# Kernel optimization log

Measured on AMD Instinct MI355X. Metric: run time of the kernel, lower is better.

The kernel has to match this reference:

```python
import jax, jax.numpy as jnp
import numpy as np

N_NODES = 50000
N_EDGES = 800000
F_IN, F_HID, F_OUT = 128, 256, 256


def setup_inputs() -> dict:
    key = jax.random.key(0)
    ks = jax.random.split(key, 8)
    x = jax.random.normal(ks[0], (N_NODES, F_IN), dtype=jnp.float32)
    edge_index = jax.random.randint(ks[1], (2, N_EDGES), 0, N_NODES, dtype=jnp.int64)

    def lin(k, fan_in, fan_out):
        return jax.random.normal(k, (fan_in, fan_out), dtype=jnp.float32) / np.sqrt(fan_in).astype(np.float32)

    return {
        "x": x,
        "edge_index": edge_index,
        "W1": lin(ks[2], F_IN, F_HID),  "b1": jnp.zeros((F_HID,), jnp.float32),
        "W2": lin(ks[3], F_HID, F_HID), "b2": jnp.zeros((F_HID,), jnp.float32),
        "W3": lin(ks[4], F_HID, F_OUT), "b3": jnp.zeros((F_OUT,), jnp.float32),
    }


def reference(x, edge_index, W1, b1, W2, b2, W3, b3):
    # GCN (eval mode): edge_drop and feature dropout are identity; bn=False.
    n = x.shape[0]
    loops = jnp.arange(n, dtype=edge_index.dtype)
    src = jnp.concatenate([edge_index[0], loops])  # [E+N] with self-loops
    dst = jnp.concatenate([edge_index[1], loops])

    # Symmetric normalization deg^{-1/2}[src] * deg^{-1/2}[dst] (deg over dst incl. self-loops)
    deg = jax.ops.segment_sum(jnp.ones_like(dst, dtype=x.dtype), dst, num_segments=n)
    dinv = jnp.where(deg > 0, jax.lax.rsqrt(deg), jnp.zeros_like(deg))
    norm = dinv[src] * dinv[dst]  # [E+N]

    def gcn_conv(h, W, b):
        h = h @ W                                       # [N, out]
        msg = h[src] * norm[:, None]                    # gather + scale  [E+N, out]
        return jax.ops.segment_sum(msg, dst, num_segments=n) + b  # scatter-add

    h = jax.nn.relu(gcn_conv(x, W1, b1))
    h = jax.nn.relu(gcn_conv(h, W2, b2))
    return gcn_conv(h, W3, b3)
```

## Files before the change

kernel.cpp:

```cpp
#include <hip/hip_runtime.h>
#include <hip/hip_bf16.h>

#define NNODES 50000
#define NEDGES 800000
#define F_IN 128
#define F_HID 256

using u16 = unsigned short;
using u32 = unsigned int;
using f32x4 = __attribute__((ext_vector_type(4))) float;
using s16x8 = __attribute__((ext_vector_type(8))) short;

constexpr int SCAN_BLOCKS = (NNODES + 255) / 256;
constexpr int B2SHIFT = 9;
constexpr int NB2 = (NNODES + 511) >> 9;
constexpr int NBLK = 256;
constexpr int EPB = NEDGES / NBLK;

constexpr size_t OFF_DINV   = 0;
constexpr size_t OFF_ROWPTR = 200192;
constexpr size_t OFF_CNT    = 400384;
constexpr size_t OFF_BSUM   = 600576;
constexpr size_t OFF_BSUMS  = 601600;
constexpr size_t OFF_CMAT   = 602624;
constexpr size_t OFF_PAIRS  = 702976;
constexpr size_t OFF_PW     = 3902976;
constexpr size_t OFF_XB     = 7102976;
constexpr size_t OFF_HB     = 19902976;
constexpr size_t OFF_AGGB   = 45502976;
constexpr size_t OFF_W1T    = 71102976;
constexpr size_t OFF_W2T    = 71168512;
constexpr size_t OFF_W3T    = 71299584;

static __device__ __forceinline__ float b2f(u16 u) {
    union { unsigned int i; float f; } v;
    v.i = ((unsigned int)u) << 16;
    return v.f;
}
static __device__ __forceinline__ u16 f2b(float f) {
    __hip_bfloat16 h = __float2bfloat16(f);
    return __builtin_bit_cast(u16, h);
}

static __device__ __forceinline__ bool detect_wide(const void* raw) {
    __shared__ int bad;
    if (threadIdx.x == 0) bad = 0;
    __syncthreads();
    unsigned long long v = ((const unsigned long long*)raw)[threadIdx.x & 255];
    if (v >= (unsigned long long)NNODES) atomicAdd(&bad, 1);
    __syncthreads();
    return bad == 0;
}

__global__ __launch_bounds__(256) void hist_kernel(const void* __restrict__ raw,
                                                   int* __restrict__ cnt, int* __restrict__ cmat) {
    const bool wide = detect_wide(raw);
    __shared__ int h[NB2];
    int t = threadIdx.x;
    if (t < NB2) h[t] = 0;
    __syncthreads();
    const int base = blockIdx.x * EPB;
    for (int i = t; i < EPB; i += 256) {
        int e = base + i;
        int d = wide ? (int)((const long long*)raw)[NEDGES + e] : ((const int*)raw)[NEDGES + e];
        atomicAdd(&h[d >> B2SHIFT], 1);
        atomicAdd(&cnt[d], 1);
    }
    __syncthreads();
    if (t < NB2) cmat[t * NBLK + blockIdx.x] = h[t];
}

__global__ __launch_bounds__(256) void offset_kernel(const int* __restrict__ row_ptr, int* __restrict__ cmat) {
    __shared__ int s[256];
    int b = blockIdx.x;
    int t = threadIdx.x;
    int v = cmat[b * NBLK + t];
    s[t] = v;
    __syncthreads();
    for (int o = 1; o < 256; o <<= 1) {
        int tmp = (t >= o) ? s[t - o] : 0;
        __syncthreads();
        s[t] += tmp;
        __syncthreads();
    }
    cmat[b * NBLK + t] = row_ptr[b << B2SHIFT] + s[t] - v;
}

__global__ __launch_bounds__(256) void scatter_kernel(const void* __restrict__ raw,
                                                      const int* __restrict__ cmat,
                                                      u32* __restrict__ pairs) {
    const bool wide = detect_wide(raw);
    __shared__ int cur[NB2];
    int t = threadIdx.x;
    if (t < NB2) cur[t] = cmat[t * NBLK + blockIdx.x];
    __syncthreads();
    const int base = blockIdx.x * EPB;
    for (int i = t; i < EPB; i += 256) {
        int e = base + i;
        int s, d;
        if (wide) {
            const long long* p = (const long long*)raw;
            s = (int)p[e];
            d = (int)p[NEDGES + e];
        } else {
            const int* p = (const int*)raw;
            s = p[e];
            d = p[NEDGES + e];
        }
        int pos = atomicAdd(&cur[d >> B2SHIFT], 1);
        pairs[pos] = ((u32)(d & 511) << 16) | (u32)s;
    }
}

__global__ __launch_bounds__(256) void phase2_fill(const u32* __restrict__ pairs,
                                                   const int* __restrict__ row_ptr,
                                                   const float* __restrict__ dinv,
                                                   u32* __restrict__ pw) {
    __shared__ int lcnt[512];
    __shared__ int lbase[512];
    int b = blockIdx.x;
    int n0 = b << B2SHIFT;
    int t = threadIdx.x;
    for (int i = t; i < 512; i += 256) {
        lcnt[i] = 0;
        int nd = n0 + i;
        lbase[i] = (nd < NNODES) ? row_ptr[nd] : NEDGES;
    }
    __syncthreads();
    int hi = n0 + 512; if (hi > NNODES) hi = NNODES;
    int p0 = row_ptr[n0];
    int p1 = row_ptr[hi];
    for (int p = p0 + t; p < p1; p += 256) {
        u32 pk = pairs[p];
        int dl = (int)(pk >> 16);
        int src = (int)(pk & 0xFFFFu);
        int r = atomicAdd(&lcnt[dl], 1);
        u16 wb = f2b(dinv[src]);
        pw[lbase[dl] + r] = ((u32)wb << 16) | (u32)src;
    }
}

__global__ __launch_bounds__(256) void scan_reduce(const int* __restrict__ cnt, int* __restrict__ bsum,
                                                   float* __restrict__ dinv) {
    __shared__ int s[256];
    int i = blockIdx.x * 256 + threadIdx.x;
    int c = (i < NNODES) ? cnt[i] : 0;
    if (i < NNODES) dinv[i] = rsqrtf((float)c + 1.0f);
    s[threadIdx.x] = c;
    __syncthreads();
    for (int o = 128; o > 0; o >>= 1) {
        if (threadIdx.x < o) s[threadIdx.x] += s[threadIdx.x + o];
        __syncthreads();
    }
    if (threadIdx.x == 0) bsum[blockIdx.x] = s[0];
}

__global__ __launch_bounds__(256) void scan_top(const int* __restrict__ bsum, int* __restrict__ bsumS) {
    __shared__ int s[256];
    int t = threadIdx.x;
    int v = (t < SCAN_BLOCKS) ? bsum[t] : 0;
    s[t] = v;
    __syncthreads();
    for (int o = 1; o < 256; o <<= 1) {
        int tmp = (t >= o) ? s[t - o] : 0;
        __syncthreads();
        s[t] += tmp;
        __syncthreads();
    }
    if (t < SCAN_BLOCKS) bsumS[t] = s[t] - v;
}

__global__ __launch_bounds__(256) void scan_final(const int* __restrict__ cnt, const int* __restrict__ bsumS,
                                                  int* __restrict__ row_ptr) {
    __shared__ int s[256];
    int t = threadIdx.x;
    int i = blockIdx.x * 256 + t;
    int v = (i < NNODES) ? cnt[i] : 0;
    s[t] = v;
    __syncthreads();
    for (int o = 1; o < 256; o <<= 1) {
        int tmp = (t >= o) ? s[t - o] : 0;
        __syncthreads();
        s[t] += tmp;
        __syncthreads();
    }
    if (i < NNODES) row_ptr[i] = s[t] - v + bsumS[blockIdx.x];
    if (i == 0) row_ptr[NNODES] = NEDGES;
}

__global__ __launch_bounds__(256) void convert_all(const float* __restrict__ x,
                                                   const float* __restrict__ W1, const float* __restrict__ W2,
                                                   const float* __restrict__ W3, u16* __restrict__ xb,
                                                   u16* __restrict__ W1t, u16* __restrict__ W2t,
                                                   u16* __restrict__ W3t) {
    int bid = blockIdx.x;
    if (bid < 6250) {
        int i = bid * 256 + threadIdx.x;
        float4 v = ((const float4*)x)[i];
        ushort4 o;
        o.x = f2b(v.x); o.y = f2b(v.y); o.z = f2b(v.z); o.w = f2b(v.w);
        ((ushort4*)xb)[i] = o;
    } else {
        int idx = (bid - 6250) * 256 + threadIdx.x;
        if (idx < 32768) {
            int k = idx >> 8, n = idx & 255;
            W1t[n * 128 + k] = f2b(W1[idx]);
        } else if (idx < 98304) {
            int j = idx - 32768;
            int k = j >> 8, n = j & 255;
            W2t[n * 256 + k] = f2b(W2[j]);
        } else {
            int j = idx - 98304;
            int k = j >> 8, n = j & 255;
            W3t[n * 256 + k] = f2b(W3[j]);
        }
    }
}

template <int F>
__global__ __launch_bounds__(256) void agg_kernel(const u16* __restrict__ h,
                                                  const int* __restrict__ row_ptr,
                                                  const u32* __restrict__ pw,
                                                  const float* __restrict__ dinv,
                                                  u16* __restrict__ outb) {
    constexpr int VEC = F / 64;
    int lane = threadIdx.x & 63;
    int v = __builtin_amdgcn_readfirstlane((int)(blockIdx.x * 4 + (threadIdx.x >> 6)));
    const size_t lo = (size_t)lane * VEC;

    const int e0 = row_ptr[v], e1 = row_ptr[v + 1];
    float dv = dinv[v];
    float acc[VEC];
    {
        const u16* p = h + (size_t)v * F + lo;
        if constexpr (VEC == 4) {
            ushort4 t = *(const ushort4*)p;
            acc[0] = dv * b2f(t.x); acc[1] = dv * b2f(t.y); acc[2] = dv * b2f(t.z); acc[3] = dv * b2f(t.w);
        } else {
            ushort2 t = *(const ushort2*)p;
            acc[0] = dv * b2f(t.x); acc[1] = dv * b2f(t.y);
        }
    }
    for (int e = e0; e < e1; e += 8) {
        u32 pk[8];
#pragma unroll
        for (int u = 0; u < 8; ++u) {
            int idx = e + u;
            pk[u] = pw[idx < e1 ? idx : e1 - 1];
        }
        int   c[8];
        float w[8];
#pragma unroll
        for (int u = 0; u < 8; ++u) {
            c[u] = (int)(pk[u] & 0xFFFFu);
            w[u] = (e + u < e1) ? b2f((u16)(pk[u] >> 16)) : 0.0f;
        }
        if constexpr (VEC == 4) {
            ushort4 r[8];
#pragma unroll
            for (int u = 0; u < 8; ++u)
                r[u] = *(const ushort4*)(h + (size_t)c[u] * F + lo);
#pragma unroll
            for (int u = 0; u < 8; ++u) {
                acc[0] += w[u] * b2f(r[u].x);
                acc[1] += w[u] * b2f(r[u].y);
                acc[2] += w[u] * b2f(r[u].z);
                acc[3] += w[u] * b2f(r[u].w);
            }
        } else {
            ushort2 r[8];
#pragma unroll
            for (int u = 0; u < 8; ++u)
                r[u] = *(const ushort2*)(h + (size_t)c[u] * F + lo);
#pragma unroll
            for (int u = 0; u < 8; ++u) {
                acc[0] += w[u] * b2f(r[u].x);
                acc[1] += w[u] * b2f(r[u].y);
            }
        }
    }
    u16* o = outb + (size_t)v * F + lo;
    if constexpr (VEC == 4) {
        ushort4 t;
        t.x = f2b(dv * acc[0]); t.y = f2b(dv * acc[1]); t.z = f2b(dv * acc[2]); t.w = f2b(dv * acc[3]);
        *(ushort4*)o = t;
    } else {
        ushort2 t;
        t.x = f2b(dv * acc[0]); t.y = f2b(dv * acc[1]);
        *(ushort2*)o = t;
    }
}

template <int KT, bool RELU, bool OUT_BF16>
__global__ __launch_bounds__(256) void gemm_mfma(const u16* __restrict__ A, const u16* __restrict__ Wt,
                                                 const float* __restrict__ bias, void* __restrict__ outp,
                                                 int M) {
    constexpr int BM = 128, BN = 128, BK = 32;
    __shared__ __align__(16) u16 As[BM * BK];
    __shared__ __align__(16) u16 Bs[BN * BK];
    const int tid = threadIdx.x;
    const int lane = tid & 63, wid = tid >> 6;
    const int l15 = lane & 15, lhi = lane >> 4;
    const int m0 = blockIdx.x * BM, n0 = blockIdx.y * BN;
    const int wr = (wid >> 1) * 64, wc = (wid & 1) * 64;

    f32x4 acc[4][4] = {};

    const int sr = tid >> 1;
    const int sc2 = (tid & 1) * 2;

    for (int k0 = 0; k0 < KT; k0 += BK) {
        uint4 av0, av1, bv0, bv1;
        int ar = m0 + sr;
        if (ar < M) {
            const uint4* ap = (const uint4*)(A + (size_t)ar * KT + k0 + sc2 * 8);
            av0 = ap[0]; av1 = ap[1];
        } else {
            av0 = make_uint4(0, 0, 0, 0); av1 = av0;
        }
        const uint4* bp = (const uint4*)(Wt + (size_t)(n0 + sr) * KT + k0 + sc2 * 8);
        bv0 = bp[0]; bv1 = bp[1];

        __syncthreads();
        *(uint4*)&As[sr * BK + ((sc2 ^ (sr & 3)) * 8)]       = av0;
        *(uint4*)&As[sr * BK + (((sc2 + 1) ^ (sr & 3)) * 8)] = av1;
        *(uint4*)&Bs[sr * BK + ((sc2 ^ (sr & 3)) * 8)]       = bv0;
        *(uint4*)&Bs[sr * BK + (((sc2 + 1) ^ (sr & 3)) * 8)] = bv1;
        __syncthreads();

        s16x8 af[4], bfr[4];
#pragma unroll
        for (int m = 0; m < 4; ++m) {
            int r = wr + m * 16 + l15;
            af[m] = *(const s16x8*)&As[r * BK + ((lhi ^ (r & 3)) * 8)];
        }
#pragma unroll
        for (int n = 0; n < 4; ++n) {
            int r = wc + n * 16 + l15;
            bfr[n] = *(const s16x8*)&Bs[r * BK + ((lhi ^ (r & 3)) * 8)];
        }
#pragma unroll
        for (int m = 0; m < 4; ++m)
#pragma unroll
            for (int n = 0; n < 4; ++n)
                acc[m][n] = __builtin_amdgcn_mfma_f32_16x16x32_bf16(af[m], bfr[n], acc[m][n], 0, 0, 0);
    }

#pragma unroll
    for (int n = 0; n < 4; ++n) {
        int gcol = n0 + wc + n * 16 + l15;
        float bb = bias[gcol];
#pragma unroll
        for (int m = 0; m < 4; ++m) {
            int gr0 = m0 + wr + m * 16 + lhi * 4;
#pragma unroll
            for (int r = 0; r < 4; ++r) {
                int gr = gr0 + r;
                if (gr >= M) continue;
                float vv = acc[m][n][r] + bb;
                if (RELU) vv = vv > 0.f ? vv : 0.f;
                if (OUT_BF16)
                    ((u16*)outp)[(size_t)gr * 256 + gcol] = f2b(vv);
                else
                    ((float*)outp)[(size_t)gr * 256 + gcol] = vv;
            }
        }
    }
}

extern "C" void kernel_launch(void* const* d_in, const int* in_sizes, int n_in,
                              void* d_out, int out_size, void* d_ws, size_t ws_size,
                              hipStream_t stream) {
    const float* x  = (const float*)d_in[0];
    const void* edges = d_in[1];
    const float* W1 = (const float*)d_in[2];
    const float* b1 = (const float*)d_in[3];
    const float* W2 = (const float*)d_in[4];
    const float* b2 = (const float*)d_in[5];
    const float* W3 = (const float*)d_in[6];
    const float* b3 = (const float*)d_in[7];
    float* out = (float*)d_out;

    char* ws = (char*)d_ws;
    float* dinv   = (float*)(ws + OFF_DINV);
    int*   rowptr = (int*)(ws + OFF_ROWPTR);
    int*   cnt    = (int*)(ws + OFF_CNT);
    int*   bsum   = (int*)(ws + OFF_BSUM);
    int*   bsumS  = (int*)(ws + OFF_BSUMS);
    int*   cmat   = (int*)(ws + OFF_CMAT);
    u32*   pairs  = (u32*)(ws + OFF_PAIRS);
    u32*   pw     = (u32*)(ws + OFF_PW);
    u16*   xb     = (u16*)(ws + OFF_XB);
    u16*   hb     = (u16*)(ws + OFF_HB);
    u16*   aggb   = (u16*)(ws + OFF_AGGB);
    u16*   W1t    = (u16*)(ws + OFF_W1T);
    u16*   W2t    = (u16*)(ws + OFF_W2T);
    u16*   W3t    = (u16*)(ws + OFF_W3T);

    hipMemsetAsync(cnt, 0, NNODES * sizeof(int), stream);

    hist_kernel<<<NBLK, 256, 0, stream>>>(edges, cnt, cmat);

    scan_reduce<<<SCAN_BLOCKS, 256, 0, stream>>>(cnt, bsum, dinv);
    scan_top<<<1, 256, 0, stream>>>(bsum, bsumS);
    scan_final<<<SCAN_BLOCKS, 256, 0, stream>>>(cnt, bsumS, rowptr);

    offset_kernel<<<NB2, 256, 0, stream>>>(rowptr, cmat);
    scatter_kernel<<<NBLK, 256, 0, stream>>>(edges, cmat, pairs);
    phase2_fill<<<NB2, 256, 0, stream>>>(pairs, rowptr, dinv, pw);

    convert_all<<<6890, 256, 0, stream>>>(x, W1, W2, W3, xb, W1t, W2t, W3t);

    const int AGG_GRID = NNODES / 4;
    dim3 ggrid((NNODES + 127) / 128, 2);

    agg_kernel<F_IN><<<AGG_GRID, 256, 0, stream>>>(xb, rowptr, pw, dinv, aggb);
    gemm_mfma<F_IN, true, true><<<ggrid, 256, 0, stream>>>(aggb, W1t, b1, hb, NNODES);

    agg_kernel<F_HID><<<AGG_GRID, 256, 0, stream>>>(hb, rowptr, pw, dinv, aggb);
    gemm_mfma<F_HID, true, true><<<ggrid, 256, 0, stream>>>(aggb, W2t, b2, hb, NNODES);

    agg_kernel<F_HID><<<AGG_GRID, 256, 0, stream>>>(hb, rowptr, pw, dinv, aggb);
    gemm_mfma<F_HID, false, false><<<ggrid, 256, 0, stream>>>(aggb, W3t, b3, out, NNODES);
}
```

Measured before the change: 316.5 us.

## Derive CSR row pointers from bucket-local counts, drop global degree atomics

Removes the per-node global atomic degree histogram, its memset, and the three-kernel global scan. Row pointers and inverse sqrt degrees are now computed per 512-node bucket from the already-bucketed pairs, using shared-memory counts and a scan, and a small scan over bucket totals supplies the bucket bases. The aggregation inner loop is also unrolled from 8 to 16 edges to keep more gathers in flight, at the cost of more registers. The fill pass now needs a second read of pairs.

```diff
diff --git a/kernel.cpp b/kernel.cpp
--- a/kernel.cpp
+++ b/kernel.cpp
@@ -11,7 +11,6 @@
 using f32x4 = __attribute__((ext_vector_type(4))) float;
 using s16x8 = __attribute__((ext_vector_type(8))) short;
 
-constexpr int SCAN_BLOCKS = (NNODES + 255) / 256;
 constexpr int B2SHIFT = 9;
 constexpr int NB2 = (NNODES + 511) >> 9;
 constexpr int NBLK = 256;
@@ -19,18 +18,17 @@
 
 constexpr size_t OFF_DINV   = 0;
 constexpr size_t OFF_ROWPTR = 200192;
-constexpr size_t OFF_CNT    = 400384;
-constexpr size_t OFF_BSUM   = 600576;
-constexpr size_t OFF_BSUMS  = 601600;
-constexpr size_t OFF_CMAT   = 602624;
-constexpr size_t OFF_PAIRS  = 702976;
-constexpr size_t OFF_PW     = 3902976;
-constexpr size_t OFF_XB     = 7102976;
-constexpr size_t OFF_HB     = 19902976;
-constexpr size_t OFF_AGGB   = 45502976;
-constexpr size_t OFF_W1T    = 71102976;
-constexpr size_t OFF_W2T    = 71168512;
-constexpr size_t OFF_W3T    = 71299584;
+constexpr size_t OFF_CMAT   = 400384;
+constexpr size_t OFF_BTOT   = 500736;
+constexpr size_t OFF_BBASE  = 501760;
+constexpr size_t OFF_PAIRS  = 502784;
+constexpr size_t OFF_PW     = 3702784;
+constexpr size_t OFF_XB     = 6902784;
+constexpr size_t OFF_HB     = 19702784;
+constexpr size_t OFF_AGGB   = 45302784;
+constexpr size_t OFF_W1T    = 70902784;
+constexpr size_t OFF_W2T    = 70968320;
+constexpr size_t OFF_W3T    = 71099392;
 
 static __device__ __forceinline__ float b2f(u16 u) {
     union { unsigned int i; float f; } v;
@@ -52,8 +50,7 @@
     return bad == 0;
 }
 
-__global__ __launch_bounds__(256) void hist_kernel(const void* __restrict__ raw,
-                                                   int* __restrict__ cnt, int* __restrict__ cmat) {
+__global__ __launch_bounds__(256) void hist_kernel(const void* __restrict__ raw, int* __restrict__ cmat) {
     const bool wide = detect_wide(raw);
     __shared__ int h[NB2];
     int t = threadIdx.x;
@@ -64,13 +61,12 @@
         int e = base + i;
         int d = wide ? (int)((const long long*)raw)[NEDGES + e] : ((const int*)raw)[NEDGES + e];
         atomicAdd(&h[d >> B2SHIFT], 1);
-        atomicAdd(&cnt[d], 1);
     }
     __syncthreads();
     if (t < NB2) cmat[t * NBLK + blockIdx.x] = h[t];
 }
 
-__global__ __launch_bounds__(256) void offset_kernel(const int* __restrict__ row_ptr, int* __restrict__ cmat) {
+__global__ __launch_bounds__(256) void offset_kernel(int* __restrict__ cmat, int* __restrict__ btot) {
     __shared__ int s[256];
     int b = blockIdx.x;
     int t = threadIdx.x;
@@ -83,16 +79,33 @@
         s[t] += tmp;
         __syncthreads();
     }
-    cmat[b * NBLK + t] = row_ptr[b << B2SHIFT] + s[t] - v;
+    cmat[b * NBLK + t] = s[t] - v;
+    if (t == 255) btot[b] = s[255];
+}
+
+__global__ void bscan_kernel(const int* __restrict__ btot, int* __restrict__ bbase) {
+    __shared__ int s[128];
+    int t = threadIdx.x;
+    int v = (t < NB2) ? btot[t] : 0;
+    s[t] = v;
+    __syncthreads();
+    for (int o = 1; o < 128; o <<= 1) {
+        int tmp = (t >= o) ? s[t - o] : 0;
+        __syncthreads();
+        s[t] += tmp;
+        __syncthreads();
+    }
+    if (t < NB2) bbase[t] = s[t] - v;
 }
 
 __global__ __launch_bounds__(256) void scatter_kernel(const void* __restrict__ raw,
                                                       const int* __restrict__ cmat,
+                                                      const int* __restrict__ bbase,
                                                       u32* __restrict__ pairs) {
     const bool wide = detect_wide(raw);
     __shared__ int cur[NB2];
     int t = threadIdx.x;
-    if (t < NB2) cur[t] = cmat[t * NBLK + blockIdx.x];
+    if (t < NB2) cur[t] = cmat[t * NBLK + blockIdx.x] + bbase[t];
     __syncthreads();
     const int base = blockIdx.x * EPB;
     for (int i = t; i < EPB; i += 256) {
@@ -112,80 +125,54 @@
     }
 }
 
-__global__ __launch_bounds__(256) void phase2_fill(const u32* __restrict__ pairs,
-                                                   const int* __restrict__ row_ptr,
-                                                   const float* __restrict__ dinv,
-                                                   u32* __restrict__ pw) {
+__global__ __launch_bounds__(256) void phase2a(const u32* __restrict__ pairs,
+                                               const int* __restrict__ bbase, const int* __restrict__ btot,
+                                               int* __restrict__ row_ptr, float* __restrict__ dinv) {
     __shared__ int lcnt[512];
-    __shared__ int lbase[512];
-    int b = blockIdx.x;
+    __shared__ int ssc[512];
+    int b = blockIdx.x, t = threadIdx.x;
     int n0 = b << B2SHIFT;
-    int t = threadIdx.x;
-    for (int i = t; i < 512; i += 256) {
-        lcnt[i] = 0;
-        int nd = n0 + i;
-        lbase[i] = (nd < NNODES) ? row_ptr[nd] : NEDGES;
-    }
-    __syncthreads();
-    int hi = n0 + 512; if (hi > NNODES) hi = NNODES;
-    int p0 = row_ptr[n0];
-    int p1 = row_ptr[hi];
+    lcnt[t] = 0; lcnt[t + 256] = 0;
+    __syncthreads();
+    int p0 = bbase[b], p1 = p0 + btot[b];
+    for (int p = p0 + t; p < p1; p += 256)
+        atomicAdd(&lcnt[pairs[p] >> 16], 1);
+    __syncthreads();
+    int c0 = lcnt[t], c1 = lcnt[t + 256];
+    ssc[t] = c0; ssc[t + 256] = c1;
+    __syncthreads();
+    for (int o = 1; o < 512; o <<= 1) {
+        int a0 = (t >= o) ? ssc[t - o] : 0;
+        int a1 = ssc[t + 256 - o];
+        __syncthreads();
+        ssc[t] += a0; ssc[t + 256] += a1;
+        __syncthreads();
+    }
+    int na = n0 + t, nb = n0 + t + 256;
+    if (na < NNODES) { row_ptr[na] = p0 + ssc[t] - c0;       dinv[na] = rsqrtf((float)c0 + 1.0f); }
+    if (nb < NNODES) { row_ptr[nb] = p0 + ssc[t + 256] - c1; dinv[nb] = rsqrtf((float)c1 + 1.0f); }
+    if (b == 0 && t == 0) row_ptr[NNODES] = NEDGES;
+}
+
+__global__ __launch_bounds__(256) void phase2b(const u32* __restrict__ pairs,
+                                               const int* __restrict__ bbase, const int* __restrict__ btot,
+                                               const int* __restrict__ row_ptr, const float* __restrict__ dinv,
+                                               u32* __restrict__ pw) {
+    __shared__ int lcur[512];
+    int b = blockIdx.x, t = threadIdx.x;
+    int n0 = b << B2SHIFT;
+    int na = n0 + t, nb = n0 + t + 256;
+    lcur[t]       = (na < NNODES) ? row_ptr[na] : NEDGES;
+    lcur[t + 256] = (nb < NNODES) ? row_ptr[nb] : NEDGES;
+    __syncthreads();
+    int p0 = bbase[b], p1 = p0 + btot[b];
     for (int p = p0 + t; p < p1; p += 256) {
         u32 pk = pairs[p];
         int dl = (int)(pk >> 16);
         int src = (int)(pk & 0xFFFFu);
-        int r = atomicAdd(&lcnt[dl], 1);
-        u16 wb = f2b(dinv[src]);
-        pw[lbase[dl] + r] = ((u32)wb << 16) | (u32)src;
-    }
-}
-
-__global__ __launch_bounds__(256) void scan_reduce(const int* __restrict__ cnt, int* __restrict__ bsum,
-                                                   float* __restrict__ dinv) {
-    __shared__ int s[256];
-    int i = blockIdx.x * 256 + threadIdx.x;
-    int c = (i < NNODES) ? cnt[i] : 0;
-    if (i < NNODES) dinv[i] = rsqrtf((float)c + 1.0f);
-    s[threadIdx.x] = c;
-    __syncthreads();
-    for (int o = 128; o > 0; o >>= 1) {
-        if (threadIdx.x < o) s[threadIdx.x] += s[threadIdx.x + o];
-        __syncthreads();
-    }
-    if (threadIdx.x == 0) bsum[blockIdx.x] = s[0];
-}
-
-__global__ __launch_bounds__(256) void scan_top(const int* __restrict__ bsum, int* __restrict__ bsumS) {
-    __shared__ int s[256];
-    int t = threadIdx.x;
-    int v = (t < SCAN_BLOCKS) ? bsum[t] : 0;
-    s[t] = v;
-    __syncthreads();
-    for (int o = 1; o < 256; o <<= 1) {
-        int tmp = (t >= o) ? s[t - o] : 0;
-        __syncthreads();
-        s[t] += tmp;
-        __syncthreads();
-    }
-    if (t < SCAN_BLOCKS) bsumS[t] = s[t] - v;
-}
-
-__global__ __launch_bounds__(256) void scan_final(const int* __restrict__ cnt, const int* __restrict__ bsumS,
-                                                  int* __restrict__ row_ptr) {
-    __shared__ int s[256];
-    int t = threadIdx.x;
-    int i = blockIdx.x * 256 + t;
-    int v = (i < NNODES) ? cnt[i] : 0;
-    s[t] = v;
-    __syncthreads();
-    for (int o = 1; o < 256; o <<= 1) {
-        int tmp = (t >= o) ? s[t - o] : 0;
-        __syncthreads();
-        s[t] += tmp;
-        __syncthreads();
-    }
-    if (i < NNODES) row_ptr[i] = s[t] - v + bsumS[blockIdx.x];
-    if (i == 0) row_ptr[NNODES] = NEDGES;
+        int pos = atomicAdd(&lcur[dl], 1);
+        pw[pos] = ((u32)f2b(dinv[src]) << 16) | (u32)src;
+    }
 }
 
 __global__ __launch_bounds__(256) void convert_all(const float* __restrict__ x,
@@ -241,39 +228,39 @@
             acc[0] = dv * b2f(t.x); acc[1] = dv * b2f(t.y);
         }
     }
-    for (int e = e0; e < e1; e += 8) {
-        u32 pk[8];
-#pragma unroll
-        for (int u = 0; u < 8; ++u) {
+    for (int e = e0; e < e1; e += 16) {
+        u32 pk[16];
+#pragma unroll
+        for (int u = 0; u < 16; ++u) {
             int idx = e + u;
             pk[u] = pw[idx < e1 ? idx : e1 - 1];
         }
-        int   c[8];
-        float w[8];
-#pragma unroll
-        for (int u = 0; u < 8; ++u) {
+        int   c[16];
+        float w[16];
+#pragma unroll
+        for (int u = 0; u < 16; ++u) {
             c[u] = (int)(pk[u] & 0xFFFFu);
             w[u] = (e + u < e1) ? b2f((u16)(pk[u] >> 16)) : 0.0f;
         }
         if constexpr (VEC == 4) {
-            ushort4 r[8];
-#pragma unroll
-            for (int u = 0; u < 8; ++u)
+            ushort4 r[16];
+#pragma unroll
+            for (int u = 0; u < 16; ++u)
                 r[u] = *(const ushort4*)(h + (size_t)c[u] * F + lo);
 #pragma unroll
-            for (int u = 0; u < 8; ++u) {
+            for (int u = 0; u < 16; ++u) {
                 acc[0] += w[u] * b2f(r[u].x);
                 acc[1] += w[u] * b2f(r[u].y);
                 acc[2] += w[u] * b2f(r[u].z);
                 acc[3] += w[u] * b2f(r[u].w);
             }
         } else {
-            ushort2 r[8];
-#pragma unroll
-            for (int u = 0; u < 8; ++u)
+            ushort2 r[16];
+#pragma unroll
+            for (int u = 0; u < 16; ++u)
                 r[u] = *(const ushort2*)(h + (size_t)c[u] * F + lo);
 #pragma unroll
-            for (int u = 0; u < 8; ++u) {
+            for (int u = 0; u < 16; ++u) {
                 acc[0] += w[u] * b2f(r[u].x);
                 acc[1] += w[u] * b2f(r[u].y);
             }
@@ -384,10 +371,9 @@
     char* ws = (char*)d_ws;
     float* dinv   = (float*)(ws + OFF_DINV);
     int*   rowptr = (int*)(ws + OFF_ROWPTR);
-    int*   cnt    = (int*)(ws + OFF_CNT);
-    int*   bsum   = (int*)(ws + OFF_BSUM);
-    int*   bsumS  = (int*)(ws + OFF_BSUMS);
     int*   cmat   = (int*)(ws + OFF_CMAT);
+    int*   btot   = (int*)(ws + OFF_BTOT);
+    int*   bbase  = (int*)(ws + OFF_BBASE);
     u32*   pairs  = (u32*)(ws + OFF_PAIRS);
     u32*   pw     = (u32*)(ws + OFF_PW);
     u16*   xb     = (u16*)(ws + OFF_XB);
@@ -397,17 +383,12 @@
     u16*   W2t    = (u16*)(ws + OFF_W2T);
     u16*   W3t    = (u16*)(ws + OFF_W3T);
 
-    hipMemsetAsync(cnt, 0, NNODES * sizeof(int), stream);
-
-    hist_kernel<<<NBLK, 256, 0, stream>>>(edges, cnt, cmat);
-
-    scan_reduce<<<SCAN_BLOCKS, 256, 0, stream>>>(cnt, bsum, dinv);
-    scan_top<<<1, 256, 0, stream>>>(bsum, bsumS);
-    scan_final<<<SCAN_BLOCKS, 256, 0, stream>>>(cnt, bsumS, rowptr);
-
-    offset_kernel<<<NB2, 256, 0, stream>>>(rowptr, cmat);
-    scatter_kernel<<<NBLK, 256, 0, stream>>>(edges, cmat, pairs);
-    phase2_fill<<<NB2, 256, 0, stream>>>(pairs, rowptr, dinv, pw);
+    hist_kernel<<<NBLK, 256, 0, stream>>>(edges, cmat);
+    offset_kernel<<<NB2, 256, 0, stream>>>(cmat, btot);
+    bscan_kernel<<<1, 128, 0, stream>>>(btot, bbase);
+    scatter_kernel<<<NBLK, 256, 0, stream>>>(edges, cmat, bbase, pairs);
+    phase2a<<<NB2, 256, 0, stream>>>(pairs, bbase, btot, rowptr, dinv);
+    phase2b<<<NB2, 256, 0, stream>>>(pairs, bbase, btot, rowptr, dinv, pw);
 
     convert_all<<<6890, 256, 0, stream>>>(x, W1, W2, W3, xb, W1t, W2t, W3t);
 
```

After: 283.4 us. 10.5% less time.
